# Kernel optimization log

Measured on AMD Instinct MI355X. Metric: run time of the kernel, lower is better.

The kernel has to match this reference:

```python
import jax, jax.numpy as jnp
import numpy as np
from jax.ops import segment_sum, segment_max

N = 100000   # nodes
E = 800000   # edges (avg degree 8, spatial KNN graph)
IN, HID, OUT = 256, 128, 32
K_SMOOTH = (2, 2)  # num_smooth_iterations


def setup_inputs() -> dict:
    key = jax.random.key(0)
    ks = jax.random.split(key, 16)
    def p(k, shape, s=0.1):
        return jax.random.normal(k, shape, jnp.float32) * s
    return {
        "features": jax.random.normal(ks[0], (N, IN), jnp.float32),
        "edge_index": jax.random.randint(ks[1], (2, E), 0, N),
        "W1s": p(ks[2], (IN, HID)), "W1d": p(ks[3], (IN, HID)),
        "a1s": p(ks[4], (HID,)), "a1d": p(ks[5], (HID,)),
        "W2s": p(ks[6], (HID, OUT)), "W2d": p(ks[7], (HID, OUT)),
        "a2s": p(ks[8], (OUT,)), "a2d": p(ks[9], (OUT,)),
        "a3s": p(ks[10], (HID,)), "a3d": p(ks[11], (HID,)),
        "a4s": p(ks[12], (IN,)), "a4d": p(ks[13], (IN,)),
        "alpha1": jnp.float32(0.5),
        "alpha2": jnp.float32(0.5),
    }


def gat(x, src, dst, Ws, Wd, a_s, a_d, n, attention):
    # single-head GATConv, concat=False, no self loops, no bias
    xs = x @ Ws            # [N, out]
    xd = x @ Wd            # [N, out]
    msg = xs[src]          # [E, out] edge-wise gather
    if attention:
        s = jax.nn.leaky_relu((xs @ a_s)[src] + (xd @ a_d)[dst], 0.2)  # [E]
        mx = segment_max(s, dst, num_segments=n)
        e = jnp.exp(s - mx[dst])
        den = segment_sum(e, dst, num_segments=n)
        w = e / den[dst]   # softmax over incoming edges of each dst node
    else:
        deg = segment_sum(jnp.ones_like(src, dtype=x.dtype), dst, num_segments=n)
        w = 1.0 / deg[dst]  # uniform attention == mean aggregation
    return segment_sum(w[:, None] * msg, dst, num_segments=n)  # [N, out]


def _forward(features, edge_index, W1s, W1d, a1s, a1d, W2s, W2d, a2s, a2d,
             a3s, a3d, a4s, a4d, alpha1, alpha2):
    n = features.shape[0]
    src, dst = edge_index[0], edge_index[1]

    h1 = jax.nn.selu(gat(features, src, dst, W1s, W1d, a1s, a1d, n, True))
    h2 = gat(h1, src, dst, W2s, W2d, a2s, a2d, n, True)
    # decoder ties weights: conv3 = conv2^T, conv4 = conv1^T
    h3 = jax.nn.selu(gat(h2, src, dst, W2s.T, W2d.T, a3s, a3d, n, True))
    h4 = gat(h3, src, dst, W1s.T, W1d.T, a4s, a4d, n, False)

    # learnable smoothing (deg from row=src, exponent -0.6)
    ones = jnp.ones_like(src, dtype=features.dtype)
    deg = segment_sum(ones, src, num_segments=n)
    dis = jnp.where(deg > 0, deg ** -0.6, 0.0)
    n1 = dis[src] * dis[dst] * alpha1
    n2 = dis[src] * dis[dst] * alpha2 * 2.0
    s1 = h2
    s2 = h2
    for _ in range(K_SMOOTH[0]):
        s1 = segment_sum(n1[:, None] * s1[dst], src, num_segments=n)  # adj1 @ s1
        s2 = segment_sum(n2[:, None] * s2[dst], src, num_segments=n)  # adj2 @ s2
    sm = 0.5 * s1 + 0.5 * s2

    # dynamic smoothing (exponent -0.5, degree-dependent alpha)
    dis2 = jnp.where(deg > 0, deg ** -0.5, 0.0)
    al = 1.0 / (1.0 + jnp.log(deg + 1.0))
    norm = dis2[src] * dis2[dst] * al[src]
    for _ in range(K_SMOOTH[1]):
        sm = segment_sum(norm[:, None] * sm[dst], src, num_segments=n)
    return sm, h4


def reference(features, edge_index, W1s, W1d, a1s, a1d, W2s, W2d, a2s, a2d,
              a3s, a3d, a4s, a4d, alpha1, alpha2):
    return _forward(features, edge_index, W1s, W1d, a1s, a1d, W2s, W2d,
                    a2s, a2d, a3s, a3d, a4s, a4d, alpha1, alpha2)
```

## Files before the change

### kernel.cpp

```cpp
#include <hip/hip_runtime.h>


#define SELU_S 1.0507009873554805f
#define SELU_A 1.6732632423543772f

typedef short bf16x8 __attribute__((ext_vector_type(8)));
typedef float f32x4 __attribute__((ext_vector_type(4)));

__device__ __forceinline__ float selu_f(float v){
  return v > 0.f ? SELU_S * v : SELU_S * SELU_A * (__expf(v) - 1.f);
}
__device__ __forceinline__ float b2f(unsigned short u){
  return __uint_as_float((unsigned)u << 16);
}
__device__ __forceinline__ unsigned short f2b(float f){
  unsigned u = __float_as_uint(f);
  u += 0x7fffu + ((u >> 16) & 1u);
  return (unsigned short)(u >> 16);
}
__device__ __forceinline__ void gload_lds16(const void* g, void* l){
  __builtin_amdgcn_global_load_lds(
      (const __attribute__((address_space(1))) unsigned int*)g,
      (__attribute__((address_space(3))) unsigned int*)l, 16, 0, 0);
}

__global__ __launch_bounds__(256) void prep_weights(
    const float* __restrict__ W1s, const float* __restrict__ W2s,
    unsigned short* __restrict__ W1sT_h, unsigned short* __restrict__ W1s_h,
    unsigned short* __restrict__ W2sT_h, unsigned short* __restrict__ W2s_h){
  int t = blockIdx.x * 256 + threadIdx.x;
  if (t < 32768){
    W1s_h[t] = f2b(W1s[t]);
    int k = t / 256, d = t % 256;
    W1sT_h[t] = f2b(W1s[d * 128 + k]);
  }
  if (t < 4096){
    W2s_h[t] = f2b(W2s[t]);
    int k = t / 128, d = t % 128;
    W2sT_h[t] = f2b(W2s[d * 32 + k]);
  }
}

__global__ __launch_bounds__(256) void cvt_dots(
    const float* __restrict__ X, unsigned short* __restrict__ Xh,
    const float* __restrict__ u1, const float* __restrict__ v1,
    float* __restrict__ p, float* __restrict__ q, int N){
  int g = blockIdx.x * 256 + threadIdx.x;
  int node = g >> 6, lane = g & 63;
  if (node >= N) return;
  float4 x = *reinterpret_cast<const float4*>(X + (size_t)node * 256 + lane * 4);
  uint2 r;
  r.x = (unsigned)f2b(x.x) | ((unsigned)f2b(x.y) << 16);
  r.y = (unsigned)f2b(x.z) | ((unsigned)f2b(x.w) << 16);
  *reinterpret_cast<uint2*>(Xh + (size_t)node * 256 + lane * 4) = r;
  float4 uu = *reinterpret_cast<const float4*>(u1 + lane * 4);
  float4 vv = *reinterpret_cast<const float4*>(v1 + lane * 4);
  float s1 = x.x*uu.x + x.y*uu.y + x.z*uu.z + x.w*uu.w;
  float s2 = x.x*vv.x + x.y*vv.y + x.z*vv.z + x.w*vv.w;
  for (int m = 32; m; m >>= 1){ s1 += __shfl_xor(s1, m); s2 += __shfl_xor(s2, m); }
  if (lane == 0){ p[node] = s1; q[node] = s2; }
}

__global__ void precompute_vecs(const float* __restrict__ W1s, const float* __restrict__ W1d,
                                const float* __restrict__ a1s, const float* __restrict__ a1d,
                                const float* __restrict__ W2s, const float* __restrict__ W2d,
                                const float* __restrict__ a2s, const float* __restrict__ a2d,
                                const float* __restrict__ a3s, const float* __restrict__ a3d,
                                float* u1, float* v1, float* u2, float* v2,
                                float* u3, float* v3,
                                const float* alpha1, const float* alpha2, float* sscale){
  int t = threadIdx.x;
  float s1 = 0.f, s2 = 0.f;
  for (int j = 0; j < 128; j++){ s1 += W1s[t*128+j]*a1s[j]; s2 += W1d[t*128+j]*a1d[j]; }
  u1[t] = s1; v1[t] = s2;
  if (t < 128){
    float s3 = 0.f, s4 = 0.f;
    for (int j = 0; j < 32; j++){ s3 += W2s[t*32+j]*a2s[j]; s4 += W2d[t*32+j]*a2d[j]; }
    u2[t] = s3; v2[t] = s4;
  }
  if (t < 32){
    float s5 = 0.f, s6 = 0.f;
    for (int j = 0; j < 128; j++){ s5 += W2s[j*32+t]*a3s[j]; s6 += W2d[j*32+t]*a3d[j]; }
    u3[t] = s5; v3[t] = s6;
  }
  if (t == 0){
    float a = alpha1[0], b = alpha2[0];
    sscale[0] = 0.5f * (a*a + 4.f*b*b);
  }
}


__global__ __launch_bounds__(256) void bucket_hist(
    const int* __restrict__ src, const int* __restrict__ dst,
    int* __restrict__ bcntD, int* __restrict__ bcntS, int E){
  __shared__ int hD[256], hS[256];
  int tid = threadIdx.x;
  hD[tid] = 0; hS[tid] = 0;
  __syncthreads();
  int base = blockIdx.x * 4096;
  for (int i = 0; i < 16; i++){
    int e = base + tid + i * 256;
    if (e < E){
      atomicAdd(&hD[dst[e] >> 9], 1);
      atomicAdd(&hS[src[e] >> 9], 1);
    }
  }
  __syncthreads();
  if (hD[tid]) atomicAdd(&bcntD[tid], hD[tid]);
  if (hS[tid]) atomicAdd(&bcntS[tid], hS[tid]);
}

__global__ void bucket_scan(const int* __restrict__ bcntD, const int* __restrict__ bcntS,
                            int* bbaseD, int* bbaseS, int* bcurD, int* bcurS, int NBK){
  __shared__ int t1[256], t2[256];
  int tid = threadIdx.x;
  int v1 = (tid < NBK) ? bcntD[tid] : 0;
  int v2 = (tid < NBK) ? bcntS[tid] : 0;
  t1[tid] = v1; t2[tid] = v2;
  __syncthreads();
  for (int off = 1; off < 256; off <<= 1){
    int a1 = (tid >= off) ? t1[tid - off] : 0;
    int a2 = (tid >= off) ? t2[tid - off] : 0;
    __syncthreads();
    t1[tid] += a1; t2[tid] += a2;
    __syncthreads();
  }
  int e1 = t1[tid] - v1, e2 = t2[tid] - v2;
  bbaseD[tid] = e1; bcurD[tid] = e1;
  bbaseS[tid] = e2; bcurS[tid] = e2;
  if (tid == NBK - 1){ bbaseD[NBK] = t1[tid]; bbaseS[NBK] = t2[tid]; }
}

__global__ __launch_bounds__(256) void bin_stage(
    const int* __restrict__ src, const int* __restrict__ dst,
    int* __restrict__ bcurD, int* __restrict__ bcurS,
    unsigned* __restrict__ stgD, unsigned* __restrict__ stgS, int E){
  __shared__ int hD[256], hS[256], bD[256], bS[256];
  int tid = threadIdx.x;
  hD[tid] = 0; hS[tid] = 0;
  __syncthreads();
  int base = blockIdx.x * 4096;
  int s[16], d[16];
  for (int i = 0; i < 16; i++){
    int e = base + tid + i * 256;
    if (e < E){
      s[i] = src[e]; d[i] = dst[e];
      atomicAdd(&hD[d[i] >> 9], 1);
      atomicAdd(&hS[s[i] >> 9], 1);
    } else s[i] = -1;
  }
  __syncthreads();
  bD[tid] = hD[tid] ? atomicAdd(&bcurD[tid], hD[tid]) : 0;
  bS[tid] = hS[tid] ? atomicAdd(&bcurS[tid], hS[tid]) : 0;
  hD[tid] = 0; hS[tid] = 0;
  __syncthreads();
  for (int i = 0; i < 16; i++){
    if (s[i] < 0) continue;
    int kb = d[i] >> 9;
    int pos = bD[kb] + atomicAdd(&hD[kb], 1);
    stgD[pos] = ((unsigned)(d[i] & 511) << 17) | (unsigned)s[i];
    kb = s[i] >> 9;
    pos = bS[kb] + atomicAdd(&hS[kb], 1);
    stgS[pos] = ((unsigned)(s[i] & 511) << 17) | (unsigned)d[i];
  }
}

__global__ __launch_bounds__(256) void place_csr(
    const unsigned* __restrict__ stgD, const unsigned* __restrict__ stgS,
    const int* __restrict__ bbaseD, const int* __restrict__ bbaseS,
    int* __restrict__ adjD, int* __restrict__ adjS,
    int* __restrict__ degD, int* __restrict__ offD,
    int* __restrict__ degS, int* __restrict__ offS,
    float* __restrict__ dis, float* __restrict__ pna, float* __restrict__ qn,
    int N, int NBK){
  bool isS = blockIdx.x >= (unsigned)NBK;
  int b = isS ? blockIdx.x - NBK : blockIdx.x;
  const unsigned* stg = isS ? stgS : stgD;
  const int* bbase = isS ? bbaseS : bbaseD;
  int* adj = isS ? adjS : adjD;
  int* deg = isS ? degS : degD;
  int* off = isS ? offS : offD;
  int n0 = b << 9;
  int r0 = bbase[b], r1 = bbase[b + 1];

  __shared__ int cnt[512];
  __shared__ int exc[512];
  __shared__ int tmp[256];
  int tid = threadIdx.x;
  cnt[2*tid] = 0; cnt[2*tid + 1] = 0;
  __syncthreads();
  for (int i = r0 + tid; i < r1; i += 256) atomicAdd(&cnt[stg[i] >> 17], 1);
  __syncthreads();
  int c0 = cnt[2*tid], c1 = cnt[2*tid + 1];
  int ts = c0 + c1;
  tmp[tid] = ts;
  __syncthreads();
  for (int o2 = 1; o2 < 256; o2 <<= 1){
    int a = (tid >= o2) ? tmp[tid - o2] : 0;
    __syncthreads();
    tmp[tid] += a;
    __syncthreads();
  }
  int e0 = tmp[tid] - ts;
  exc[2*tid] = e0; exc[2*tid + 1] = e0 + c0;
  __syncthreads();
  for (int l = tid; l < 512; l += 256){
    int n = n0 + l;
    if (n < N){
      deg[n] = cnt[l];
      off[n] = r0 + exc[l];
      if (isS){
        float dd = (float)cnt[l];
        float di = dd > 0.f ? powf(dd, -0.6f) : 0.f;
        float d2 = dd > 0.f ? powf(dd, -0.5f) : 0.f;
        float al = 1.f / (1.f + logf(dd + 1.f));
        dis[n] = di; pna[n] = d2 * al; qn[n] = d2;
      }
    }
  }
  __syncthreads();
  for (int l = tid; l < 512; l += 256) cnt[l] = r0 + exc[l];
  __syncthreads();
  for (int i = r0 + tid; i < r1; i += 256){
    unsigned p = stg[i];
    int pos = atomicAdd(&cnt[p >> 17], 1);
    adj[pos] = (int)(p & 0x1FFFFu);
  }
}

template<int DIM, int G, bool ATTN, bool DO_SELU, bool OUT_BF16, bool DOTS>
__global__ __launch_bounds__(256) void fused_gat(
    const int* __restrict__ off, const int* __restrict__ degs, const int* __restrict__ adj,
    const float* __restrict__ ps, const float* __restrict__ pd,
    const unsigned short* __restrict__ xin, void* __restrict__ out_,
    const float* __restrict__ un, const float* __restrict__ vn,
    float* __restrict__ psn, float* __restrict__ pdn_o, int N){
  constexpr int R = DIM / G;
  static_assert(R == 2, "R must be 2");
  int t = blockIdx.x * 256 + threadIdx.x;
  int node = t / G;
  int gl = t % G;
  if (node >= N) return;
  int base = (threadIdx.x & 63) & ~(G - 1);
  int o = off[node], dg = degs[node];
  float acc0 = 0.f, acc1 = 0.f;

  auto ldu = [&](int nj) -> uint {
    return *reinterpret_cast<const uint*>(xin + (size_t)nj * DIM + gl * 2);
  };
  auto accum = [&](uint u, float wj){
    acc0 += wj * __uint_as_float(u << 16);
    acc1 += wj * __uint_as_float(u & 0xffff0000u);
  };

  if (ATTN){
    float pdn = pd[node];
    if (dg <= G){
      int nid = 0;
      float s = -1e30f;
      if (gl < dg){
        nid = adj[o + gl];
        s = ps[nid] + pdn;
        s = s > 0.f ? s : 0.2f * s;
      }
      float m = s;
      for (int msk = G >> 1; msk; msk >>= 1) m = fmaxf(m, __shfl_xor(m, msk));
      float e = (gl < dg) ? __expf(s - m) : 0.f;
      float den = e;
      for (int msk = G >> 1; msk; msk >>= 1) den += __shfl_xor(den, msk);
      float w = (dg > 0) ? e / den : 0.f;
      int j = 0;
      for (; j + 8 <= dg; j += 8){
        int   n0 = __shfl(nid, base+j),   n1 = __shfl(nid, base+j+1);
        int   n2 = __shfl(nid, base+j+2), n3 = __shfl(nid, base+j+3);
        int   n4 = __shfl(nid, base+j+4), n5 = __shfl(nid, base+j+5);
        int   n6 = __shfl(nid, base+j+6), n7 = __shfl(nid, base+j+7);
        float w0 = __shfl(w, base+j),     w1 = __shfl(w, base+j+1);
        float w2 = __shfl(w, base+j+2),   w3 = __shfl(w, base+j+3);
        float w4 = __shfl(w, base+j+4),   w5 = __shfl(w, base+j+5);
        float w6 = __shfl(w, base+j+6),   w7 = __shfl(w, base+j+7);
        uint u0 = ldu(n0), u1 = ldu(n1), u2 = ldu(n2), u3 = ldu(n3);
        uint u4 = ldu(n4), u5 = ldu(n5), u6 = ldu(n6), u7 = ldu(n7);
        accum(u0, w0); accum(u1, w1); accum(u2, w2); accum(u3, w3);
        accum(u4, w4); accum(u5, w5); accum(u6, w6); accum(u7, w7);
      }
      for (; j + 4 <= dg; j += 4){
        int   n0 = __shfl(nid, base+j),   n1 = __shfl(nid, base+j+1);
        int   n2 = __shfl(nid, base+j+2), n3 = __shfl(nid, base+j+3);
        float w0 = __shfl(w, base+j),     w1 = __shfl(w, base+j+1);
        float w2 = __shfl(w, base+j+2),   w3 = __shfl(w, base+j+3);
        uint u0 = ldu(n0), u1 = ldu(n1), u2 = ldu(n2), u3 = ldu(n3);
        accum(u0, w0); accum(u1, w1); accum(u2, w2); accum(u3, w3);
      }
      for (; j < dg; j++){
        int nj = __shfl(nid, base+j);
        float wj = __shfl(w, base+j);
        accum(ldu(nj), wj);
      }
    } else {
      float m = -1e30f;
      for (int k = gl; k < dg; k += G){
        float s = ps[adj[o + k]] + pdn;
        s = s > 0.f ? s : 0.2f * s;
        m = fmaxf(m, s);
      }
      for (int msk = G >> 1; msk; msk >>= 1) m = fmaxf(m, __shfl_xor(m, msk));
      float den = 0.f;
      for (int k = gl; k < dg; k += G){
        float s = ps[adj[o + k]] + pdn;
        s = s > 0.f ? s : 0.2f * s;
        den += __expf(s - m);
      }
      for (int msk = G >> 1; msk; msk >>= 1) den += __shfl_xor(den, msk);
      float inv = 1.f / den;
      for (int c0 = 0; c0 < dg; c0 += G){
        int cn = min(G, dg - c0);
        int nid = 0; float w = 0.f;
        if (gl < cn){
          nid = adj[o + c0 + gl];
          float s = ps[nid] + pdn;
          s = s > 0.f ? s : 0.2f * s;
          w = __expf(s - m) * inv;
        }
        for (int j = 0; j < cn; j++){
          float wj = __shfl(w, base + j);
          int   nj = __shfl(nid, base + j);
          accum(ldu(nj), wj);
        }
      }
    }
  } else {
    for (int c0 = 0; c0 < dg; c0 += G){
      int cn = min(G, dg - c0);
      int nid = (gl < cn) ? adj[o + c0 + gl] : 0;
      int j = 0;
      for (; j + 8 <= cn; j += 8){
        int n0 = __shfl(nid, base+j),   n1 = __shfl(nid, base+j+1);
        int n2 = __shfl(nid, base+j+2), n3 = __shfl(nid, base+j+3);
        int n4 = __shfl(nid, base+j+4), n5 = __shfl(nid, base+j+5);
        int n6 = __shfl(nid, base+j+6), n7 = __shfl(nid, base+j+7);
        uint u0 = ldu(n0), u1 = ldu(n1), u2 = ldu(n2), u3 = ldu(n3);
        uint u4 = ldu(n4), u5 = ldu(n5), u6 = ldu(n6), u7 = ldu(n7);
        accum(u0, 1.f); accum(u1, 1.f); accum(u2, 1.f); accum(u3, 1.f);
        accum(u4, 1.f); accum(u5, 1.f); accum(u6, 1.f); accum(u7, 1.f);
      }
      for (; j + 4 <= cn; j += 4){
        int n0 = __shfl(nid, base+j),   n1 = __shfl(nid, base+j+1);
        int n2 = __shfl(nid, base+j+2), n3 = __shfl(nid, base+j+3);
        uint u0 = ldu(n0), u1 = ldu(n1), u2 = ldu(n2), u3 = ldu(n3);
        accum(u0, 1.f); accum(u1, 1.f); accum(u2, 1.f); accum(u3, 1.f);
      }
      for (; j < cn; j++){
        int nj = __shfl(nid, base + j);
        accum(ldu(nj), 1.f);
      }
    }
    float inv = dg > 0 ? 1.f / (float)dg : 0.f;
    acc0 *= inv; acc1 *= inv;
  }
  if (DO_SELU){ acc0 = selu_f(acc0); acc1 = selu_f(acc1); }
  if (DOTS){
    float s1 = acc0 * un[gl*2] + acc1 * un[gl*2+1];
    float s2 = acc0 * vn[gl*2] + acc1 * vn[gl*2+1];
    for (int msk = G >> 1; msk; msk >>= 1){ s1 += __shfl_xor(s1, msk); s2 += __shfl_xor(s2, msk); }
    if (gl == 0){ psn[node] = s1; pdn_o[node] = s2; }
  }
  if (OUT_BF16){
    unsigned short* out = (unsigned short*)out_;
    uint u = (uint)f2b(acc0) | ((uint)f2b(acc1) << 16);
    *reinterpret_cast<uint*>(out + (size_t)node * DIM + gl * 2) = u;
  } else {
    float* out = (float*)out_;
    out[(size_t)node * DIM + gl*2] = acc0;
    out[(size_t)node * DIM + gl*2 + 1] = acc1;
  }
}

template<bool OUT_B>
__global__ __launch_bounds__(256) void fused_smooth(
    const int* __restrict__ off, const int* __restrict__ degs, const int* __restrict__ adj,
    const float* __restrict__ pn, const float* __restrict__ qn,
    const float* __restrict__ scale,
    const unsigned short* __restrict__ xin, void* __restrict__ out_, int N){
  const int G = 16;
  int t = blockIdx.x * 256 + threadIdx.x;
  int node = t / G, gl = t % G;
  if (node >= N) return;
  int base = (threadIdx.x & 63) & ~(G - 1);
  int o = off[node], dg = degs[node];
  float pnv = pn[node] * (scale ? scale[0] : 1.f);
  float acc0 = 0.f, acc1 = 0.f;
  auto ldu = [&](int nj) -> uint {
    return *reinterpret_cast<const uint*>(xin + (size_t)nj * 32 + gl * 2);
  };
  for (int c0 = 0; c0 < dg; c0 += G){
    int cn = min(G, dg - c0);
    int nid = 0; float qv = 0.f;
    if (gl < cn){ nid = adj[o + c0 + gl]; qv = qn[nid]; }
    int j = 0;
    for (; j + 8 <= cn; j += 8){
      int   n0 = __shfl(nid, base+j),   n1 = __shfl(nid, base+j+1);
      int   n2 = __shfl(nid, base+j+2), n3 = __shfl(nid, base+j+3);
      int   n4 = __shfl(nid, base+j+4), n5 = __shfl(nid, base+j+5);
      int   n6 = __shfl(nid, base+j+6), n7 = __shfl(nid, base+j+7);
      float q0 = __shfl(qv, base+j),    q1 = __shfl(qv, base+j+1);
      float q2 = __shfl(qv, base+j+2),  q3 = __shfl(qv, base+j+3);
      float q4 = __shfl(qv, base+j+4),  q5 = __shfl(qv, base+j+5);
      float q6 = __shfl(qv, base+j+6),  q7 = __shfl(qv, base+j+7);
      uint u0 = ldu(n0), u1 = ldu(n1), u2 = ldu(n2), u3 = ldu(n3);
      uint u4 = ldu(n4), u5 = ldu(n5), u6 = ldu(n6), u7 = ldu(n7);
      acc0 += q0 * __uint_as_float(u0 << 16); acc1 += q0 * __uint_as_float(u0 & 0xffff0000u);
      acc0 += q1 * __uint_as_float(u1 << 16); acc1 += q1 * __uint_as_float(u1 & 0xffff0000u);
      acc0 += q2 * __uint_as_float(u2 << 16); acc1 += q2 * __uint_as_float(u2 & 0xffff0000u);
      acc0 += q3 * __uint_as_float(u3 << 16); acc1 += q3 * __uint_as_float(u3 & 0xffff0000u);
      acc0 += q4 * __uint_as_float(u4 << 16); acc1 += q4 * __uint_as_float(u4 & 0xffff0000u);
      acc0 += q5 * __uint_as_float(u5 << 16); acc1 += q5 * __uint_as_float(u5 & 0xffff0000u);
      acc0 += q6 * __uint_as_float(u6 << 16); acc1 += q6 * __uint_as_float(u6 & 0xffff0000u);
      acc0 += q7 * __uint_as_float(u7 << 16); acc1 += q7 * __uint_as_float(u7 & 0xffff0000u);
    }
    for (; j + 4 <= cn; j += 4){
      int   n0 = __shfl(nid, base+j),   n1 = __shfl(nid, base+j+1);
      int   n2 = __shfl(nid, base+j+2), n3 = __shfl(nid, base+j+3);
      float q0 = __shfl(qv, base+j),    q1 = __shfl(qv, base+j+1);
      float q2 = __shfl(qv, base+j+2),  q3 = __shfl(qv, base+j+3);
      uint u0 = ldu(n0), u1 = ldu(n1), u2 = ldu(n2), u3 = ldu(n3);
      acc0 += q0 * __uint_as_float(u0 << 16); acc1 += q0 * __uint_as_float(u0 & 0xffff0000u);
      acc0 += q1 * __uint_as_float(u1 << 16); acc1 += q1 * __uint_as_float(u1 & 0xffff0000u);
      acc0 += q2 * __uint_as_float(u2 << 16); acc1 += q2 * __uint_as_float(u2 & 0xffff0000u);
      acc0 += q3 * __uint_as_float(u3 << 16); acc1 += q3 * __uint_as_float(u3 & 0xffff0000u);
    }
    for (; j < cn; j++){
      int   nj = __shfl(nid, base + j);
      float wj = __shfl(qv,  base + j);
      uint u = ldu(nj);
      acc0 += wj * __uint_as_float(u << 16);
      acc1 += wj * __uint_as_float(u & 0xffff0000u);
    }
  }
  acc0 *= pnv; acc1 *= pnv;
  if (OUT_B){
    uint u = (uint)f2b(acc0) | ((uint)f2b(acc1) << 16);
    *reinterpret_cast<uint*>((unsigned short*)out_ + (size_t)node * 32 + gl * 2) = u;
  } else {
    float2 v; v.x = acc0; v.y = acc1;
    *reinterpret_cast<float2*>((float*)out_ + (size_t)node * 32 + gl * 2) = v;
  }
}

template<int D, int K, int CB, bool DO_SELU, bool OUT_BF16>
__global__ __launch_bounds__(256) void gemm_mfma(
    const unsigned short* __restrict__ A, const unsigned short* __restrict__ Bt,
    void* __restrict__ Cout, int M){
  constexpr int NF = CB / 16;
  int wave = threadIdx.x >> 6;
  int lane = threadIdx.x & 63;
  int row0 = blockIdx.x * 64 + wave * 16;
  int col0 = blockIdx.y * CB;
  int l15 = lane & 15;
  int arow = row0 + l15;
  int g8 = (lane >> 4) * 8;
  bool rowok = arow < M;
  f32x4 acc[NF] = {};
  for (int k0 = 0; k0 < D; k0 += 32){
    bf16x8 a = {};
    if (rowok) a = *reinterpret_cast<const bf16x8*>(A + (size_t)arow * D + k0 + g8);
    #pragma unroll
    for (int f = 0; f < NF; f++){
      bf16x8 b = *reinterpret_cast<const bf16x8*>(
          Bt + (size_t)(col0 + f * 16 + l15) * D + k0 + g8);
      acc[f] = __builtin_amdgcn_mfma_f32_16x16x32_bf16(b, a, acc[f], 0, 0, 0);
    }
  }
  if (!rowok) return;
  int cb = (lane >> 4) * 4;
  #pragma unroll
  for (int f = 0; f < NF; f++){
    float v0 = acc[f][0], v1 = acc[f][1], v2 = acc[f][2], v3 = acc[f][3];
    if (DO_SELU){ v0 = selu_f(v0); v1 = selu_f(v1); v2 = selu_f(v2); v3 = selu_f(v3); }
    size_t idx = (size_t)arow * K + col0 + f * 16 + cb;
    if (OUT_BF16){
      uint2 u;
      u.x = (uint)f2b(v0) | ((uint)f2b(v1) << 16);
      u.y = (uint)f2b(v2) | ((uint)f2b(v3) << 16);
      *reinterpret_cast<uint2*>((unsigned short*)Cout + idx) = u;
    } else {
      f32x4 v = { v0, v1, v2, v3 };
      __builtin_nontemporal_store(v, reinterpret_cast<f32x4*>((float*)Cout + idx));
    }
  }
}

template<int D, int K, bool DO_SELU, bool OUT_BF16>
__global__ __launch_bounds__(256) void gemm_pipe(
    const unsigned short* __restrict__ A, const unsigned short* __restrict__ Bt,
    void* __restrict__ Cout, int M){
  constexpr int NK = D / 32;
  constexpr int NF = K / 32;
  constexpr int AG = 2 * NK;
  constexpr int BG = 2 * NF * NK;
  extern __shared__ unsigned short smem[];
  unsigned short* Bs  = smem;
  unsigned short* As0 = smem + (size_t)K * D;
  unsigned short* As1 = As0 + 32 * D;

  const int w = threadIdx.x >> 6;
  const int lane = threadIdx.x & 63;
  const int rw = w & 1, cw = w >> 1;
  const int l15 = lane & 15, lhi = lane >> 4;

  for (int g = w; g < BG; g += 4){
    int k = g % NK, ff = g / NK;
    gload_lds16(Bt + (size_t)(ff * 16 + l15) * D + k * 32 + lhi * 8,
                Bs + (size_t)g * 512);
  }

  const int ntiles = M / 32;
  const int stride = gridDim.x;
  int t = blockIdx.x;

  auto stageA = [&](unsigned short* dstp, int tile){
    int row0 = tile * 32;
    for (int g = w; g < AG; g += 4){
      int k = g % NK, rr = g / NK;
      gload_lds16(A + (size_t)(row0 + rr * 16 + l15) * D + k * 32 + lhi * 8,
                  dstp + (size_t)g * 512);
    }
  };

  if (t < ntiles) stageA(As0, t);
  __syncthreads();

  int cur = 0;
  for (; t < ntiles; t += stride){
    unsigned short* curA = cur ? As1 : As0;
    unsigned short* nxtA = cur ? As0 : As1;
    int tn = t + stride;
    if (tn < ntiles) stageA(nxtA, tn);

    f32x4 acc[NF] = {};
    const unsigned short* Aw = curA + (size_t)rw * NK * 512;
    #pragma unroll
    for (int k = 0; k < NK; k++){
      bf16x8 a = *reinterpret_cast<const bf16x8*>(Aw + ((size_t)k * 64 + lane) * 8);
      #pragma unroll
      for (int f = 0; f < NF; f++){
        bf16x8 b = *reinterpret_cast<const bf16x8*>(
            Bs + (((size_t)(cw * NF + f) * NK + k) * 64 + lane) * 8);
        acc[f] = __builtin_amdgcn_mfma_f32_16x16x32_bf16(b, a, acc[f], 0, 0, 0);
      }
    }
    int row = t * 32 + rw * 16 + l15;
    #pragma unroll
    for (int f = 0; f < NF; f++){
      float v0 = acc[f][0], v1 = acc[f][1], v2 = acc[f][2], v3 = acc[f][3];
      if (DO_SELU){ v0 = selu_f(v0); v1 = selu_f(v1); v2 = selu_f(v2); v3 = selu_f(v3); }
      size_t idx = (size_t)row * K + cw * (K / 2) + f * 16 + lhi * 4;
      if (OUT_BF16){
        uint2 u;
        u.x = (uint)f2b(v0) | ((uint)f2b(v1) << 16);
        u.y = (uint)f2b(v2) | ((uint)f2b(v3) << 16);
        *reinterpret_cast<uint2*>((unsigned short*)Cout + idx) = u;
      } else {
        f32x4 v = { v0, v1, v2, v3 };
        __builtin_nontemporal_store(v, reinterpret_cast<f32x4*>((float*)Cout + idx));
      }
    }
    __syncthreads();
    cur ^= 1;
  }
}

extern "C" void kernel_launch(void* const* d_in, const int* in_sizes, int n_in,
                              void* d_out, int out_size, void* d_ws, size_t ws_size,
                              hipStream_t stream){
  const float* X    = (const float*)d_in[0];
  const int*   eidx = (const int*)d_in[1];
  const float* W1s  = (const float*)d_in[2];
  const float* W1d  = (const float*)d_in[3];
  const float* a1s  = (const float*)d_in[4];
  const float* a1d  = (const float*)d_in[5];
  const float* W2s  = (const float*)d_in[6];
  const float* W2d  = (const float*)d_in[7];
  const float* a2s  = (const float*)d_in[8];
  const float* a2d  = (const float*)d_in[9];
  const float* a3s  = (const float*)d_in[10];
  const float* a3d  = (const float*)d_in[11];
  const float* alpha1 = (const float*)d_in[14];
  const float* alpha2 = (const float*)d_in[15];

  const int N = in_sizes[0] / 256;
  const int E = in_sizes[1] / 2;
  const int* src = eidx;
  const int* dst = eidx + E;
  const int NBK = (N + 511) >> 9;

  float* out_sm = (float*)d_out;
  float* out_h4 = (float*)d_out + (size_t)N * 32;

  float* ws = (float*)d_ws;
  size_t o = 0;
  unsigned short* Xh  = (unsigned short*)(ws + o); o += (size_t)N * 128;
  unsigned short* B1h = (unsigned short*)(ws + o); o += (size_t)N * 64;
  unsigned short* H1h = (unsigned short*)(ws + o); o += (size_t)N * 64;
  unsigned short* B3h = (unsigned short*)(ws + o); o += (size_t)N * 16;
  unsigned short* H2h = (unsigned short*)(ws + o); o += (size_t)N * 16;
  unsigned short* AGG3h = (unsigned short*)(ws + o); o += (size_t)N * 16;
  unsigned short* T1h = (unsigned short*)(ws + o); o += (size_t)N * 16;
  unsigned short* T2h = (unsigned short*)(ws + o); o += (size_t)N * 16;
  float* ps_a = ws + o; o += N;
  float* pd_a = ws + o; o += N;
  float* ps_b = ws + o; o += N;
  float* pd_b = ws + o; o += N;
  int* deg_in  = (int*)(ws + o); o += N;
  int* deg_src = (int*)(ws + o); o += N;
  int* off_dst = (int*)(ws + o); o += N;
  int* off_src = (int*)(ws + o); o += N;
  int* adj_dst = (int*)(ws + o); o += E;
  int* adj_src = (int*)(ws + o); o += E;
  unsigned* stgD = (unsigned*)(ws + o); o += E;
  unsigned* stgS = (unsigned*)(ws + o); o += E;
  int* bcntD  = (int*)(ws + o); o += 256;
  int* bcntS  = (int*)(ws + o); o += 256;
  int* bbaseD = (int*)(ws + o); o += 260;
  int* bbaseS = (int*)(ws + o); o += 260;
  int* bcurD  = (int*)(ws + o); o += 260;
  int* bcurS  = (int*)(ws + o); o += 260;
  float* dis = ws + o; o += N;
  float* pna = ws + o; o += N;
  float* qn  = ws + o; o += N;
  unsigned short* W1sT_h = (unsigned short*)(ws + o); o += 128 * 256 / 2;
  unsigned short* W2sT_h = (unsigned short*)(ws + o); o += 32 * 128 / 2;
  unsigned short* W2s_h  = (unsigned short*)(ws + o); o += 128 * 32 / 2;
  unsigned short* W1s_h  = (unsigned short*)(ws + o); o += 256 * 128 / 2;
  float* u1 = ws + o; o += 256;
  float* v1 = ws + o; o += 256;
  float* u2 = ws + o; o += 128;
  float* v2 = ws + o; o += 128;
  float* u3 = ws + o; o += 32;
  float* v3 = ws + o; o += 32;
  float* sscale = ws + o; o += 1;

  const int TPB = 256;
  const int EBLK = (E + 4095) / 4096;
  const int RB = (N + 63) / 64;
  auto blocksFor = [](size_t n){ return (unsigned)((n + 255) / 256); };

  precompute_vecs<<<1, 256, 0, stream>>>(W1s, W1d, a1s, a1d, W2s, W2d, a2s, a2d,
                                         a3s, a3d, u1, v1, u2, v2, u3, v3,
                                         alpha1, alpha2, sscale);
  prep_weights<<<128, 256, 0, stream>>>(W1s, W2s, W1sT_h, W1s_h, W2sT_h, W2s_h);
  cvt_dots<<<blocksFor((size_t)N * 64), TPB, 0, stream>>>(X, Xh, u1, v1, ps_a, pd_a, N);

  (void)hipMemsetAsync(bcntD, 0, 512 * 4, stream);
  bucket_hist<<<EBLK, TPB, 0, stream>>>(src, dst, bcntD, bcntS, E);
  bucket_scan<<<1, 256, 0, stream>>>(bcntD, bcntS, bbaseD, bbaseS, bcurD, bcurS, NBK);
  bin_stage<<<EBLK, TPB, 0, stream>>>(src, dst, bcurD, bcurS, stgD, stgS, E);
  place_csr<<<2 * NBK, TPB, 0, stream>>>(stgD, stgS, bbaseD, bbaseS,
                                         adj_dst, adj_src, deg_in, off_dst,
                                         deg_src, off_src, dis, pna, qn, N, NBK);

  {
    size_t lds = ((size_t)128 * 256 + 2 * 32 * 256) * 2;
    gemm_pipe<256, 128, false, true><<<256, TPB, lds, stream>>>(Xh, W1sT_h, B1h, N);
  }
  fused_gat<128, 64, true, true, true, true><<<blocksFor((size_t)N * 64), TPB, 0, stream>>>(
      off_dst, deg_in, adj_dst, ps_a, pd_a, B1h, H1h, u2, v2, ps_b, pd_b, N);

  { dim3 g(RB, 1); gemm_mfma<128, 32, 32, false, true><<<g, TPB, 0, stream>>>(H1h, W2sT_h, B3h, N); }
  fused_gat<32, 16, true, false, true, true><<<blocksFor((size_t)N * 16), TPB, 0, stream>>>(
      off_dst, deg_in, adj_dst, ps_b, pd_b, B3h, H2h, u3, v3, ps_a, pd_a, N);

  fused_gat<32, 16, true, false, true, false><<<blocksFor((size_t)N * 16), TPB, 0, stream>>>(
      off_dst, deg_in, adj_dst, ps_a, pd_a, H2h, AGG3h, nullptr, nullptr, nullptr, nullptr, N);
  { dim3 g(RB, 2); gemm_mfma<32, 128, 64, true, true><<<g, TPB, 0, stream>>>(AGG3h, W2s_h, B1h, N); }

  fused_gat<128, 64, false, false, true, false><<<blocksFor((size_t)N * 64), TPB, 0, stream>>>(
      off_dst, deg_in, adj_dst, nullptr, nullptr, B1h, H1h, nullptr, nullptr, nullptr, nullptr, N);
  {
    size_t lds = ((size_t)256 * 128 + 2 * 32 * 128) * 2;
    gemm_pipe<128, 256, false, false><<<512, TPB, lds, stream>>>(H1h, W1s_h, out_h4, N);
  }

  fused_smooth<true><<<blocksFor((size_t)N * 16), TPB, 0, stream>>>(
      off_src, deg_src, adj_src, dis, dis, nullptr, H2h, T1h, N);
  fused_smooth<true><<<blocksFor((size_t)N * 16), TPB, 0, stream>>>(
      off_src, deg_src, adj_src, dis, dis, sscale, T1h, T2h, N);
  fused_smooth<true><<<blocksFor((size_t)N * 16), TPB, 0, stream>>>(
      off_src, deg_src, adj_src, pna, qn, nullptr, T2h, T1h, N);
  fused_smooth<false><<<blocksFor((size_t)N * 16), TPB, 0, stream>>>(
      off_src, deg_src, adj_src, pna, qn, nullptr, T1h, out_sm, N);
}
```

Measured before the change: 413.1 us.

## Use fewer lanes per node with wider vector loads in GAT and smoothing

Generalizes fused_gat to handle several elements per lane (8 for the 128-wide layers) with uint2/uint4 vector loads, and launches it with 16 lanes per node instead of 64. The smoothing kernel now uses 8 lanes per node with 4 elements each. The chunked attention path also gets batched 8/4 gathers. The aim is to cut shuffle and softmax overhead per node, give more nodes per wave, and issue wider memory transactions. In exchange, nodes with degree above the group size need more softmax chunks, and each lane uses more registers.

```diff
diff --git a/kernel.cpp b/kernel.cpp
--- a/kernel.cpp
+++ b/kernel.cpp
@@ -18,6 +18,18 @@
   u += 0x7fffu + ((u >> 16) & 1u);
   return (unsigned short)(u >> 16);
 }
+__device__ __forceinline__ unsigned packbf(float a, float b){
+  return (unsigned)f2b(a) | ((unsigned)f2b(b) << 16);
+}
+__device__ __forceinline__ void unpack_acc(float* acc, unsigned u, float w){
+  acc[0] += w * __uint_as_float(u << 16);
+  acc[1] += w * __uint_as_float(u & 0xffff0000u);
+}
+template<int R> struct VecT;
+template<> struct VecT<2>{ using type = unsigned int; };
+template<> struct VecT<4>{ using type = uint2; };
+template<> struct VecT<8>{ using type = uint4; };
+
 __device__ __forceinline__ void gload_lds16(const void* g, void* l){
   __builtin_amdgcn_global_load_lds(
       (const __attribute__((address_space(1))) unsigned int*)g,
@@ -50,8 +62,8 @@
   if (node >= N) return;
   float4 x = *reinterpret_cast<const float4*>(X + (size_t)node * 256 + lane * 4);
   uint2 r;
-  r.x = (unsigned)f2b(x.x) | ((unsigned)f2b(x.y) << 16);
-  r.y = (unsigned)f2b(x.z) | ((unsigned)f2b(x.w) << 16);
+  r.x = packbf(x.x, x.y);
+  r.y = packbf(x.z, x.w);
   *reinterpret_cast<uint2*>(Xh + (size_t)node * 256 + lane * 4) = r;
   float4 uu = *reinterpret_cast<const float4*>(u1 + lane * 4);
   float4 vv = *reinterpret_cast<const float4*>(v1 + lane * 4);
@@ -88,7 +100,6 @@
     sscale[0] = 0.5f * (a*a + 4.f*b*b);
   }
 }
-
 
 __global__ __launch_bounds__(256) void bucket_hist(
     const int* __restrict__ src, const int* __restrict__ dst,
@@ -236,21 +247,45 @@
     const float* __restrict__ un, const float* __restrict__ vn,
     float* __restrict__ psn, float* __restrict__ pdn_o, int N){
   constexpr int R = DIM / G;
-  static_assert(R == 2, "R must be 2");
+  using V = typename VecT<R>::type;
   int t = blockIdx.x * 256 + threadIdx.x;
   int node = t / G;
   int gl = t % G;
   if (node >= N) return;
   int base = (threadIdx.x & 63) & ~(G - 1);
   int o = off[node], dg = degs[node];
-  float acc0 = 0.f, acc1 = 0.f;
-
-  auto ldu = [&](int nj) -> uint {
-    return *reinterpret_cast<const uint*>(xin + (size_t)nj * DIM + gl * 2);
+  float acc[R] = {};
+
+  auto ldv = [&](int nj) -> V {
+    return *reinterpret_cast<const V*>(xin + (size_t)nj * DIM + gl * R);
   };
-  auto accum = [&](uint u, float wj){
-    acc0 += wj * __uint_as_float(u << 16);
-    acc1 += wj * __uint_as_float(u & 0xffff0000u);
+  auto vacc = [&](V u, float wj){
+    if constexpr (R == 2){
+      unpack_acc(acc, u, wj);
+    } else if constexpr (R == 4){
+      unpack_acc(acc, u.x, wj); unpack_acc(acc + 2, u.y, wj);
+    } else {
+      unpack_acc(acc, u.x, wj); unpack_acc(acc + 2, u.y, wj);
+      unpack_acc(acc + 4, u.z, wj); unpack_acc(acc + 6, u.w, wj);
+    }
+  };
+  auto batch8 = [&](int nid, float w, int j){
+    int nn[8]; float ww[8]; V uu[8];
+    #pragma unroll
+    for (int q = 0; q < 8; q++){ nn[q] = __shfl(nid, base + j + q); ww[q] = __shfl(w, base + j + q); }
+    #pragma unroll
+    for (int q = 0; q < 8; q++) uu[q] = ldv(nn[q]);
+    #pragma unroll
+    for (int q = 0; q < 8; q++) vacc(uu[q], ww[q]);
+  };
+  auto batch4 = [&](int nid, float w, int j){
+    int nn[4]; float ww[4]; V uu[4];
+    #pragma unroll
+    for (int q = 0; q < 4; q++){ nn[q] = __shfl(nid, base + j + q); ww[q] = __shfl(w, base + j + q); }
+    #pragma unroll
+    for (int q = 0; q < 4; q++) uu[q] = ldv(nn[q]);
+    #pragma unroll
+    for (int q = 0; q < 4; q++) vacc(uu[q], ww[q]);
   };
 
   if (ATTN){
@@ -270,32 +305,12 @@
       for (int msk = G >> 1; msk; msk >>= 1) den += __shfl_xor(den, msk);
       float w = (dg > 0) ? e / den : 0.f;
       int j = 0;
-      for (; j + 8 <= dg; j += 8){
-        int   n0 = __shfl(nid, base+j),   n1 = __shfl(nid, base+j+1);
-        int   n2 = __shfl(nid, base+j+2), n3 = __shfl(nid, base+j+3);
-        int   n4 = __shfl(nid, base+j+4), n5 = __shfl(nid, base+j+5);
-        int   n6 = __shfl(nid, base+j+6), n7 = __shfl(nid, base+j+7);
-        float w0 = __shfl(w, base+j),     w1 = __shfl(w, base+j+1);
-        float w2 = __shfl(w, base+j+2),   w3 = __shfl(w, base+j+3);
-        float w4 = __shfl(w, base+j+4),   w5 = __shfl(w, base+j+5);
-        float w6 = __shfl(w, base+j+6),   w7 = __shfl(w, base+j+7);
-        uint u0 = ldu(n0), u1 = ldu(n1), u2 = ldu(n2), u3 = ldu(n3);
-        uint u4 = ldu(n4), u5 = ldu(n5), u6 = ldu(n6), u7 = ldu(n7);
-        accum(u0, w0); accum(u1, w1); accum(u2, w2); accum(u3, w3);
-        accum(u4, w4); accum(u5, w5); accum(u6, w6); accum(u7, w7);
-      }
-      for (; j + 4 <= dg; j += 4){
-        int   n0 = __shfl(nid, base+j),   n1 = __shfl(nid, base+j+1);
-        int   n2 = __shfl(nid, base+j+2), n3 = __shfl(nid, base+j+3);
-        float w0 = __shfl(w, base+j),     w1 = __shfl(w, base+j+1);
-        float w2 = __shfl(w, base+j+2),   w3 = __shfl(w, base+j+3);
-        uint u0 = ldu(n0), u1 = ldu(n1), u2 = ldu(n2), u3 = ldu(n3);
-        accum(u0, w0); accum(u1, w1); accum(u2, w2); accum(u3, w3);
-      }
+      for (; j + 8 <= dg; j += 8) batch8(nid, w, j);
+      for (; j + 4 <= dg; j += 4) batch4(nid, w, j);
       for (; j < dg; j++){
-        int nj = __shfl(nid, base+j);
-        float wj = __shfl(w, base+j);
-        accum(ldu(nj), wj);
+        int nj = __shfl(nid, base + j);
+        float wj = __shfl(w, base + j);
+        vacc(ldv(nj), wj);
       }
     } else {
       float m = -1e30f;
@@ -322,10 +337,13 @@
           s = s > 0.f ? s : 0.2f * s;
           w = __expf(s - m) * inv;
         }
-        for (int j = 0; j < cn; j++){
+        int j = 0;
+        for (; j + 8 <= cn; j += 8) batch8(nid, w, j);
+        for (; j + 4 <= cn; j += 4) batch4(nid, w, j);
+        for (; j < cn; j++){
+          int nj = __shfl(nid, base + j);
           float wj = __shfl(w, base + j);
-          int   nj = __shfl(nid, base + j);
-          accum(ldu(nj), wj);
+          vacc(ldv(nj), wj);
         }
       }
     }
@@ -333,46 +351,50 @@
     for (int c0 = 0; c0 < dg; c0 += G){
       int cn = min(G, dg - c0);
       int nid = (gl < cn) ? adj[o + c0 + gl] : 0;
+      float w1 = 1.f;
       int j = 0;
-      for (; j + 8 <= cn; j += 8){
-        int n0 = __shfl(nid, base+j),   n1 = __shfl(nid, base+j+1);
-        int n2 = __shfl(nid, base+j+2), n3 = __shfl(nid, base+j+3);
-        int n4 = __shfl(nid, base+j+4), n5 = __shfl(nid, base+j+5);
-        int n6 = __shfl(nid, base+j+6), n7 = __shfl(nid, base+j+7);
-        uint u0 = ldu(n0), u1 = ldu(n1), u2 = ldu(n2), u3 = ldu(n3);
-        uint u4 = ldu(n4), u5 = ldu(n5), u6 = ldu(n6), u7 = ldu(n7);
-        accum(u0, 1.f); accum(u1, 1.f); accum(u2, 1.f); accum(u3, 1.f);
-        accum(u4, 1.f); accum(u5, 1.f); accum(u6, 1.f); accum(u7, 1.f);
-      }
-      for (; j + 4 <= cn; j += 4){
-        int n0 = __shfl(nid, base+j),   n1 = __shfl(nid, base+j+1);
-        int n2 = __shfl(nid, base+j+2), n3 = __shfl(nid, base+j+3);
-        uint u0 = ldu(n0), u1 = ldu(n1), u2 = ldu(n2), u3 = ldu(n3);
-        accum(u0, 1.f); accum(u1, 1.f); accum(u2, 1.f); accum(u3, 1.f);
-      }
+      for (; j + 8 <= cn; j += 8) batch8(nid, w1, j);
+      for (; j + 4 <= cn; j += 4) batch4(nid, w1, j);
       for (; j < cn; j++){
         int nj = __shfl(nid, base + j);
-        accum(ldu(nj), 1.f);
+        vacc(ldv(nj), 1.f);
       }
     }
     float inv = dg > 0 ? 1.f / (float)dg : 0.f;
-    acc0 *= inv; acc1 *= inv;
-  }
-  if (DO_SELU){ acc0 = selu_f(acc0); acc1 = selu_f(acc1); }
+    #pragma unroll
+    for (int r = 0; r < R; r++) acc[r] *= inv;
+  }
+  if (DO_SELU){
+    #pragma unroll
+    for (int r = 0; r < R; r++) acc[r] = selu_f(acc[r]);
+  }
   if (DOTS){
-    float s1 = acc0 * un[gl*2] + acc1 * un[gl*2+1];
-    float s2 = acc0 * vn[gl*2] + acc1 * vn[gl*2+1];
+    float s1 = 0.f, s2 = 0.f;
+    #pragma unroll
+    for (int r = 0; r < R; r++){
+      s1 += acc[r] * un[gl * R + r];
+      s2 += acc[r] * vn[gl * R + r];
+    }
     for (int msk = G >> 1; msk; msk >>= 1){ s1 += __shfl_xor(s1, msk); s2 += __shfl_xor(s2, msk); }
     if (gl == 0){ psn[node] = s1; pdn_o[node] = s2; }
   }
   if (OUT_BF16){
     unsigned short* out = (unsigned short*)out_;
-    uint u = (uint)f2b(acc0) | ((uint)f2b(acc1) << 16);
-    *reinterpret_cast<uint*>(out + (size_t)node * DIM + gl * 2) = u;
+    if constexpr (R == 2){
+      *reinterpret_cast<unsigned*>(out + (size_t)node * DIM + gl * 2) = packbf(acc[0], acc[1]);
+    } else if constexpr (R == 4){
+      uint2 u; u.x = packbf(acc[0], acc[1]); u.y = packbf(acc[2], acc[3]);
+      *reinterpret_cast<uint2*>(out + (size_t)node * DIM + gl * 4) = u;
+    } else {
+      uint4 u;
+      u.x = packbf(acc[0], acc[1]); u.y = packbf(acc[2], acc[3]);
+      u.z = packbf(acc[4], acc[5]); u.w = packbf(acc[6], acc[7]);
+      *reinterpret_cast<uint4*>(out + (size_t)node * DIM + gl * 8) = u;
+    }
   } else {
     float* out = (float*)out_;
-    out[(size_t)node * DIM + gl*2] = acc0;
-    out[(size_t)node * DIM + gl*2 + 1] = acc1;
+    #pragma unroll
+    for (int r = 0; r < R; r++) out[(size_t)node * DIM + gl * R + r] = acc[r];
   }
 }
 
@@ -382,68 +404,46 @@
     const float* __restrict__ pn, const float* __restrict__ qn,
     const float* __restrict__ scale,
     const unsigned short* __restrict__ xin, void* __restrict__ out_, int N){
-  const int G = 16;
+  const int G = 8;
   int t = blockIdx.x * 256 + threadIdx.x;
   int node = t / G, gl = t % G;
   if (node >= N) return;
   int base = (threadIdx.x & 63) & ~(G - 1);
   int o = off[node], dg = degs[node];
   float pnv = pn[node] * (scale ? scale[0] : 1.f);
-  float acc0 = 0.f, acc1 = 0.f;
-  auto ldu = [&](int nj) -> uint {
-    return *reinterpret_cast<const uint*>(xin + (size_t)nj * 32 + gl * 2);
+  float acc[4] = {};
+  auto ldv = [&](int nj) -> uint2 {
+    return *reinterpret_cast<const uint2*>(xin + (size_t)nj * 32 + gl * 4);
   };
   for (int c0 = 0; c0 < dg; c0 += G){
     int cn = min(G, dg - c0);
     int nid = 0; float qv = 0.f;
     if (gl < cn){ nid = adj[o + c0 + gl]; qv = qn[nid]; }
-    int j = 0;
-    for (; j + 8 <= cn; j += 8){
-      int   n0 = __shfl(nid, base+j),   n1 = __shfl(nid, base+j+1);
-      int   n2 = __shfl(nid, base+j+2), n3 = __shfl(nid, base+j+3);
-      int   n4 = __shfl(nid, base+j+4), n5 = __shfl(nid, base+j+5);
-      int   n6 = __shfl(nid, base+j+6), n7 = __shfl(nid, base+j+7);
-      float q0 = __shfl(qv, base+j),    q1 = __shfl(qv, base+j+1);
-      float q2 = __shfl(qv, base+j+2),  q3 = __shfl(qv, base+j+3);
-      float q4 = __shfl(qv, base+j+4),  q5 = __shfl(qv, base+j+5);
-      float q6 = __shfl(qv, base+j+6),  q7 = __shfl(qv, base+j+7);
-      uint u0 = ldu(n0), u1 = ldu(n1), u2 = ldu(n2), u3 = ldu(n3);
-      uint u4 = ldu(n4), u5 = ldu(n5), u6 = ldu(n6), u7 = ldu(n7);
-      acc0 += q0 * __uint_as_float(u0 << 16); acc1 += q0 * __uint_as_float(u0 & 0xffff0000u);
-      acc0 += q1 * __uint_as_float(u1 << 16); acc1 += q1 * __uint_as_float(u1 & 0xffff0000u);
-      acc0 += q2 * __uint_as_float(u2 << 16); acc1 += q2 * __uint_as_float(u2 & 0xffff0000u);
-      acc0 += q3 * __uint_as_float(u3 << 16); acc1 += q3 * __uint_as_float(u3 & 0xffff0000u);
-      acc0 += q4 * __uint_as_float(u4 << 16); acc1 += q4 * __uint_as_float(u4 & 0xffff0000u);
-      acc0 += q5 * __uint_as_float(u5 << 16); acc1 += q5 * __uint_as_float(u5 & 0xffff0000u);
-      acc0 += q6 * __uint_as_float(u6 << 16); acc1 += q6 * __uint_as_float(u6 & 0xffff0000u);
-      acc0 += q7 * __uint_as_float(u7 << 16); acc1 += q7 * __uint_as_float(u7 & 0xffff0000u);
-    }
-    for (; j + 4 <= cn; j += 4){
-      int   n0 = __shfl(nid, base+j),   n1 = __shfl(nid, base+j+1);
-      int   n2 = __shfl(nid, base+j+2), n3 = __shfl(nid, base+j+3);
-      float q0 = __shfl(qv, base+j),    q1 = __shfl(qv, base+j+1);
-      float q2 = __shfl(qv, base+j+2),  q3 = __shfl(qv, base+j+3);
-      uint u0 = ldu(n0), u1 = ldu(n1), u2 = ldu(n2), u3 = ldu(n3);
-      acc0 += q0 * __uint_as_float(u0 << 16); acc1 += q0 * __uint_as_float(u0 & 0xffff0000u);
-      acc0 += q1 * __uint_as_float(u1 << 16); acc1 += q1 * __uint_as_float(u1 & 0xffff0000u);
-      acc0 += q2 * __uint_as_float(u2 << 16); acc1 += q2 * __uint_as_float(u2 & 0xffff0000u);
-      acc0 += q3 * __uint_as_float(u3 << 16); acc1 += q3 * __uint_as_float(u3 & 0xffff0000u);
-    }
-    for (; j < cn; j++){
-      int   nj = __shfl(nid, base + j);
-      float wj = __shfl(qv,  base + j);
-      uint u = ldu(nj);
-      acc0 += wj * __uint_as_float(u << 16);
-      acc1 += wj * __uint_as_float(u & 0xffff0000u);
-    }
-  }
-  acc0 *= pnv; acc1 *= pnv;
+    if (cn == 8){
+      int nn[8]; float ww[8]; uint2 uu[8];
+      #pragma unroll
+      for (int q = 0; q < 8; q++){ nn[q] = __shfl(nid, base + q); ww[q] = __shfl(qv, base + q); }
+      #pragma unroll
+      for (int q = 0; q < 8; q++) uu[q] = ldv(nn[q]);
+      #pragma unroll
+      for (int q = 0; q < 8; q++){ unpack_acc(acc, uu[q].x, ww[q]); unpack_acc(acc + 2, uu[q].y, ww[q]); }
+    } else {
+      for (int j = 0; j < cn; j++){
+        int nj = __shfl(nid, base + j);
+        float wj = __shfl(qv, base + j);
+        uint2 u = ldv(nj);
+        unpack_acc(acc, u.x, wj); unpack_acc(acc + 2, u.y, wj);
+      }
+    }
+  }
+  #pragma unroll
+  for (int r = 0; r < 4; r++) acc[r] *= pnv;
   if (OUT_B){
-    uint u = (uint)f2b(acc0) | ((uint)f2b(acc1) << 16);
-    *reinterpret_cast<uint*>((unsigned short*)out_ + (size_t)node * 32 + gl * 2) = u;
+    uint2 u; u.x = packbf(acc[0], acc[1]); u.y = packbf(acc[2], acc[3]);
+    *reinterpret_cast<uint2*>((unsigned short*)out_ + (size_t)node * 32 + gl * 4) = u;
   } else {
-    float2 v; v.x = acc0; v.y = acc1;
-    *reinterpret_cast<float2*>((float*)out_ + (size_t)node * 32 + gl * 2) = v;
+    float4 v; v.x = acc[0]; v.y = acc[1]; v.z = acc[2]; v.w = acc[3];
+    *reinterpret_cast<float4*>((float*)out_ + (size_t)node * 32 + gl * 4) = v;
   }
 }
 
@@ -480,8 +480,8 @@
     size_t idx = (size_t)arow * K + col0 + f * 16 + cb;
     if (OUT_BF16){
       uint2 u;
-      u.x = (uint)f2b(v0) | ((uint)f2b(v1) << 16);
-      u.y = (uint)f2b(v2) | ((uint)f2b(v3) << 16);
+      u.x = packbf(v0, v1);
+      u.y = packbf(v2, v3);
       *reinterpret_cast<uint2*>((unsigned short*)Cout + idx) = u;
     } else {
       f32x4 v = { v0, v1, v2, v3 };
@@ -557,8 +557,8 @@
       size_t idx = (size_t)row * K + cw * (K / 2) + f * 16 + lhi * 4;
       if (OUT_BF16){
         uint2 u;
-        u.x = (uint)f2b(v0) | ((uint)f2b(v1) << 16);
-        u.y = (uint)f2b(v2) | ((uint)f2b(v3) << 16);
+        u.x = packbf(v0, v1);
+        u.y = packbf(v2, v3);
         *reinterpret_cast<uint2*>((unsigned short*)Cout + idx) = u;
       } else {
         f32x4 v = { v0, v1, v2, v3 };
@@ -663,7 +663,7 @@
     size_t lds = ((size_t)128 * 256 + 2 * 32 * 256) * 2;
     gemm_pipe<256, 128, false, true><<<256, TPB, lds, stream>>>(Xh, W1sT_h, B1h, N);
   }
-  fused_gat<128, 64, true, true, true, true><<<blocksFor((size_t)N * 64), TPB, 0, stream>>>(
+  fused_gat<128, 16, true, true, true, true><<<blocksFor((size_t)N * 16), TPB, 0, stream>>>(
       off_dst, deg_in, adj_dst, ps_a, pd_a, B1h, H1h, u2, v2, ps_b, pd_b, N);
 
   { dim3 g(RB, 1); gemm_mfma<128, 32, 32, false, true><<<g, TPB, 0, stream>>>(H1h, W2sT_h, B3h, N); }
@@ -674,19 +674,19 @@
       off_dst, deg_in, adj_dst, ps_a, pd_a, H2h, AGG3h, nullptr, nullptr, nullptr, nullptr, N);
   { dim3 g(RB, 2); gemm_mfma<32, 128, 64, true, true><<<g, TPB, 0, stream>>>(AGG3h, W2s_h, B1h, N); }
 
-  fused_gat<128, 64, false, false, true, false><<<blocksFor((size_t)N * 64), TPB, 0, stream>>>(
+  fused_gat<128, 16, false, false, true, false><<<blocksFor((size_t)N * 16), TPB, 0, stream>>>(
       off_dst, deg_in, adj_dst, nullptr, nullptr, B1h, H1h, nullptr, nullptr, nullptr, nullptr, N);
   {
     size_t lds = ((size_t)256 * 128 + 2 * 32 * 128) * 2;
     gemm_pipe<128, 256, false, false><<<512, TPB, lds, stream>>>(H1h, W1s_h, out_h4, N);
   }
 
-  fused_smooth<true><<<blocksFor((size_t)N * 16), TPB, 0, stream>>>(
+  fused_smooth<true><<<blocksFor((size_t)N * 8), TPB, 0, stream>>>(
       off_src, deg_src, adj_src, dis, dis, nullptr, H2h, T1h, N);
-  fused_smooth<true><<<blocksFor((size_t)N * 16), TPB, 0, stream>>>(
+  fused_smooth<true><<<blocksFor((size_t)N * 8), TPB, 0, stream>>>(
       off_src, deg_src, adj_src, dis, dis, sscale, T1h, T2h, N);
-  fused_smooth<true><<<blocksFor((size_t)N * 16), TPB, 0, stream>>>(
+  fused_smooth<true><<<blocksFor((size_t)N * 8), TPB, 0, stream>>>(
       off_src, deg_src, adj_src, pna, qn, nullptr, T2h, T1h, N);
-  fused_smooth<false><<<blocksFor((size_t)N * 16), TPB, 0, stream>>>(
+  fused_smooth<false><<<blocksFor((size_t)N * 8), TPB, 0, stream>>>(
       off_src, deg_src, adj_src, pna, qn, nullptr, T1h, out_sm, N);
 }
```

Result: no change. 406.4 us, median of 2 (-1.6%).
